# Optimization experiments

Measured on AMD Instinct MI355X. Metric: run time of the kernel, lower is better.

Reference implementation:

```python
import jax, jax.numpy as jnp
import numpy as np

H = 56; W = 56; WS = 7; SS = 3; NH = 6; C = 192; B = 32
T = H * W; HD = C // NH; NW = (H // WS) * (W // WS); TW = WS * WS
SCALE = HD ** -0.5


def _rel_index():
    # relative position index per WindowAttentionLayer.calculate_coordinates
    coords = np.stack(np.meshgrid(np.arange(WS), np.arange(WS), indexing='ij')).reshape(2, -1)
    rel = (coords[:, :, None] - coords[:, None, :]).transpose(1, 2, 0).astype(np.int64)
    rel[:, :, 0] += WS - 1
    rel[:, :, 1] += WS - 1
    rel[:, :, 0] *= 2 * WS - 1
    return rel.sum(-1).reshape(-1)  # [TW*TW]


def _attn_mask():
    # shifted-window attention mask, per WindowAttentionBlock.__init__
    img = np.zeros((H, W))
    slices = (slice(0, -WS), slice(-WS, -SS), slice(-SS, None))
    cnt = 0
    for hs in slices:
        for ws_ in slices:
            img[hs, ws_] = cnt
            cnt += 1
    mw = img.reshape(H // WS, WS, W // WS, WS).transpose(0, 2, 1, 3).reshape(-1, TW)
    am = mw[:, None, :] - mw[:, :, None]
    return np.where(am != 0, np.float32(-100.0), np.float32(0.0))  # [NW, TW, TW]


_REL = jnp.asarray(_rel_index())
_MASK = jnp.asarray(_attn_mask())


def _ln(x, g, b):
    m = x.mean(-1, keepdims=True)
    v = ((x - m) ** 2).mean(-1, keepdims=True)
    return (x - m) * jax.lax.rsqrt(v + 1e-5) * g + b


def setup_inputs() -> dict:
    key = jax.random.key(0)
    ks = jax.random.split(key, 8)
    s = 0.02
    return {
        'x': jax.random.normal(ks[0], (B, T, C), jnp.float32),
        'ln1_g': jnp.ones((C,), jnp.float32),
        'ln1_b': jnp.zeros((C,), jnp.float32),
        'qkv_w': jax.random.normal(ks[1], (C, 3 * C), jnp.float32) * s,
        'qkv_b': jnp.zeros((3 * C,), jnp.float32),
        'pos_bias': jax.random.normal(ks[2], ((2 * WS - 1) * (2 * WS - 1), NH), jnp.float32) * s,
        'proj_w': jax.random.normal(ks[3], (C, C), jnp.float32) * s,
        'proj_b': jnp.zeros((C,), jnp.float32),
        'ln2_g': jnp.ones((C,), jnp.float32),
        'ln2_b': jnp.zeros((C,), jnp.float32),
        'mlp_w1': jax.random.normal(ks[4], (C, 4 * C), jnp.float32) * s,
        'mlp_b1': jnp.zeros((4 * C,), jnp.float32),
        'mlp_w2': jax.random.normal(ks[5], (4 * C, C), jnp.float32) * s,
        'mlp_b2': jnp.zeros((C,), jnp.float32),
    }


def reference(x, ln1_g, ln1_b, qkv_w, qkv_b, pos_bias, proj_w, proj_b,
              ln2_g, ln2_b, mlp_w1, mlp_b1, mlp_w2, mlp_b2):
    shortcut = x
    h = _ln(x, ln1_g, ln1_b).reshape(B, H, W, C)
    h = jnp.roll(h, (-SS, -SS), axis=(1, 2))  # cyclic shift
    # window partition -> [B*NW, TW, C]
    h = h.reshape(B, H // WS, WS, W // WS, WS, C).transpose(0, 1, 3, 2, 4, 5).reshape(B * NW, TW, C)
    qkv = (h @ qkv_w + qkv_b).reshape(B * NW, TW, 3, NH, HD).transpose(2, 0, 3, 1, 4)
    q, k, v = qkv[0] * SCALE, qkv[1], qkv[2]  # [B*NW, NH, TW, HD]
    attn = jnp.einsum('nhid,nhjd->nhij', q, k)  # [B*NW, NH, TW, TW]
    bias = pos_bias[_REL].reshape(TW, TW, NH).transpose(2, 0, 1)  # [NH, TW, TW]
    attn = attn + bias[None]
    attn = (attn.reshape(B, NW, NH, TW, TW) + _MASK[None, :, None]).reshape(B * NW, NH, TW, TW)
    # NOTE: the source forward never applies softmax (self.softmax is unused) -- replicated faithfully
    o = jnp.einsum('nhij,nhjd->nhid', attn, v).transpose(0, 2, 1, 3).reshape(B * NW, TW, C)
    o = o @ proj_w + proj_b
    # window reverse + reverse shift
    o = o.reshape(B, H // WS, W // WS, WS, WS, C).transpose(0, 1, 3, 2, 4, 5).reshape(B, H, W, C)
    o = jnp.roll(o, (SS, SS), axis=(1, 2)).reshape(B, T, C)
    x1 = shortcut + o
    m = _ln(x1, ln2_g, ln2_b)
    m = jax.nn.gelu(m @ mlp_w1 + mlp_b1, approximate=False) @ mlp_w2 + mlp_b2
    return x1 + m
```

## Files before the change

### kernel.cpp

```cpp
#include <hip/hip_runtime.h>
#include <hip/hip_bf16.h>

typedef __attribute__((ext_vector_type(8))) short short8;
typedef __attribute__((ext_vector_type(4))) float floatx4;

#define SCALE_Q 0.17677669529663687f

__device__ __forceinline__ short f2bf(float f) {
  union { float f; unsigned u; } a; a.f = f;
  unsigned r = (a.u + 0x7FFFu + ((a.u >> 16) & 1u)) >> 16;
  return (short)r;
}

__global__ void transpose_w_k(const float* __restrict__ src, short* __restrict__ dst,
                              int K, int N) {
  int i = blockIdx.x * 256 + threadIdx.x;
  if (i >= N * K) return;
  int n = i / K, k = i - n * K;
  dst[i] = f2bf(src[(size_t)k * N + n]);
}

__global__ void prep_bm_k(const float* __restrict__ pos_bias, float* __restrict__ bm) {
  int i = blockIdx.x * 256 + threadIdx.x;
  if (i >= 64 * 6 * 49 * 49) return;
  int j = i % 49; int t = i / 49; int ii = t % 49; t /= 49; int h = t % 6; int w = t / 6;
  int ih = ii / 7, iw = ii - ih * 7, jh = j / 7, jw = j - jh * 7;
  int rel = (ih - jh + 6) * 13 + (iw - jw + 6);
  float v = pos_bias[rel * 6 + h];
  int wh = w >> 3, ww = w & 7;
  int ri = wh * 7 + ih, ci = ww * 7 + iw, rj = wh * 7 + jh, cj = ww * 7 + jw;
  int regi = ((ri >= 49) + (ri >= 53)) * 3 + ((ci >= 49) + (ci >= 53));
  int regj = ((rj >= 49) + (rj >= 53)) * 3 + ((cj >= 49) + (cj >= 53));
  if (regi != regj) v -= 100.0f;
  bm[i] = v;
}

template<int SHIFT>
__global__ __launch_bounds__(256) void ln_k(const float* __restrict__ x,
    const float* __restrict__ g, const float* __restrict__ bta,
    short* __restrict__ outb) {
  int wid = threadIdx.x >> 6, lane = threadIdx.x & 63;
  int r = blockIdx.x * 4 + wid;
  size_t src;
  if (SHIFT) {
    int n = r / 49, tw = r - n * 49;
    int bb = n >> 6, wdx = n & 63;
    int rh = (wdx >> 3) * 7 + tw / 7, rw = (wdx & 7) * 7 + tw % 7;
    int sh = rh + 3; if (sh >= 56) sh -= 56;
    int sw = rw + 3; if (sw >= 56) sw -= 56;
    src = ((size_t)bb * 3136 + sh * 56 + sw) * 192;
  } else {
    src = (size_t)r * 192;
  }
  const float* xr = x + src;
  float v0 = xr[lane], v1 = xr[lane + 64], v2 = xr[lane + 128];
  float s = v0 + v1 + v2, sq = v0 * v0 + v1 * v1 + v2 * v2;
  #pragma unroll
  for (int o = 32; o >= 1; o >>= 1) { s += __shfl_xor(s, o); sq += __shfl_xor(sq, o); }
  float mean = s * (1.0f / 192.0f);
  float rstd = rsqrtf(sq * (1.0f / 192.0f) - mean * mean + 1e-5f);
  short* orow = outb + (size_t)r * 192;
  orow[lane]       = f2bf((v0 - mean) * rstd * g[lane]       + bta[lane]);
  orow[lane + 64]  = f2bf((v1 - mean) * rstd * g[lane + 64]  + bta[lane + 64]);
  orow[lane + 128] = f2bf((v2 - mean) * rstd * g[lane + 128] + bta[lane + 128]);
}

template<int EPI>
__global__ __launch_bounds__(256) void gemm_k(
    const short* __restrict__ A, const short* __restrict__ Bt,
    const float* __restrict__ bias, void* __restrict__ outp,
    const void* __restrict__ aux, int N, int K) {
  __shared__ short As[128][72];
  __shared__ short Bs[64][72];
  int tid = threadIdx.x;
  int gmb = blockIdx.y * 128;
  int gnb = blockIdx.x * 64;
  int wid = tid >> 6, lane = tid & 63;
  int wm = wid >> 1, wn = wid & 1;
  int lr = lane & 15, lk = (lane >> 4) << 3, lq = (lane >> 4) << 2;
  floatx4 acc[4][2];
  #pragma unroll
  for (int i = 0; i < 4; ++i)
    #pragma unroll
    for (int j = 0; j < 2; ++j) acc[i][j] = (floatx4)(0.0f);

  for (int k0 = 0; k0 < K; k0 += 64) {
    #pragma unroll
    for (int i = 0; i < 4; ++i) {
      int u = tid + 256 * i;
      int row = u >> 3, cb = (u & 7) << 3;
      *(short8*)&As[row][cb] = *(const short8*)&A[(size_t)(gmb + row) * K + k0 + cb];
    }
    #pragma unroll
    for (int i = 0; i < 2; ++i) {
      int u = tid + 256 * i;
      int row = u >> 3, cb = (u & 7) << 3;
      *(short8*)&Bs[row][cb] = *(const short8*)&Bt[(size_t)(gnb + row) * K + k0 + cb];
    }
    __syncthreads();
    #pragma unroll
    for (int kk = 0; kk < 64; kk += 32) {
      short8 af[4], bfr[2];
      #pragma unroll
      for (int mi = 0; mi < 4; ++mi)
        af[mi] = *(const short8*)&As[wm * 64 + mi * 16 + lr][kk + lk];
      #pragma unroll
      for (int ni = 0; ni < 2; ++ni)
        bfr[ni] = *(const short8*)&Bs[wn * 32 + ni * 16 + lr][kk + lk];
      #pragma unroll
      for (int mi = 0; mi < 4; ++mi)
        #pragma unroll
        for (int ni = 0; ni < 2; ++ni)
          acc[mi][ni] = __builtin_amdgcn_mfma_f32_16x16x32_bf16(af[mi], bfr[ni], acc[mi][ni], 0, 0, 0);
    }
    __syncthreads();
  }

  #pragma unroll
  for (int mi = 0; mi < 4; ++mi) {
    #pragma unroll
    for (int ni = 0; ni < 2; ++ni) {
      #pragma unroll
      for (int r = 0; r < 4; ++r) {
        int grow = gmb + wm * 64 + mi * 16 + lq + r;
        int gcol = gnb + wn * 32 + ni * 16 + lr;
        float v = acc[mi][ni][r] + bias[gcol];
        if (EPI == 0) {
          int which = gcol / 192, rem = gcol - which * 192;
          if (which == 0) v *= SCALE_Q;
          int head = rem >> 5, d = rem & 31;
          int n = grow / 49, tw = grow - n * 49;
          ((short*)outp)[((((size_t)(n * 6 + head) * 3 + which) * 49 + tw) << 5) + d] = f2bf(v);
        } else if (EPI == 1) {
          int n = grow / 49, tw = grow - n * 49;
          int bb = n >> 6, wdx = n & 63;
          int rh = (wdx >> 3) * 7 + tw / 7, rw = (wdx & 7) * 7 + tw % 7;
          int oh = rh + 3; if (oh >= 56) oh -= 56;
          int ow = rw + 3; if (ow >= 56) ow -= 56;
          size_t idx = ((size_t)bb * 3136 + oh * 56 + ow) * 192 + gcol;
          ((float*)outp)[idx] = ((const float*)aux)[idx] + v;
        } else if (EPI == 2) {
          float ge = 0.5f * v * (1.0f + erff(v * 0.70710678118f));
          ((short*)outp)[(size_t)grow * 768 + gcol] = f2bf(ge);
        } else {
          size_t idx = (size_t)grow * 192 + gcol;
          ((float*)outp)[idx] += v;
        }
      }
    }
  }
}

__global__ __launch_bounds__(256) void attn_k(const short* __restrict__ qkv,
    const float* __restrict__ bm, short* __restrict__ obuf) {
  __shared__ short lds[4][6912];
  int wid = threadIdx.x >> 6, lane = threadIdx.x & 63;
  int pair = blockIdx.x * 4 + wid;
  int n = pair / 6, h = pair - n * 6;
  short* Vt = &lds[wid][0];
  short* Ps = &lds[wid][32 * 72];
  const short* Qb = qkv + (size_t)((n * 6 + h) * 3) * 1568;
  const short* Kb = Qb + 1568;
  const short* Vb = Qb + 3136;
  int lr = lane & 15, lk = (lane >> 4) << 3, lq = (lane >> 4) << 2;

  #pragma unroll
  for (int it = 0; it < 8; ++it) {
    int u = lane + 64 * it;
    Vt[(u >> 4) * 72 + 48 + (u & 15)] = 0;
  }
  #pragma unroll
  for (int it = 0; it < 4; ++it) {
    int u = lane + 64 * it;
    if (u < 196) {
      int tw = u >> 2, db = (u & 3) << 3;
      short8 vv = *(const short8*)&Vb[tw * 32 + db];
      #pragma unroll
      for (int j = 0; j < 8; ++j) Vt[(db + j) * 72 + tw] = vv[j];
    }
  }

  short8 qf[4], kf[4];
  #pragma unroll
  for (int mi = 0; mi < 4; ++mi)
    qf[mi] = *(const short8*)&Qb[(mi * 16 + lr) * 32 + lk];
  #pragma unroll
  for (int nj = 0; nj < 4; ++nj)
    kf[nj] = *(const short8*)&Kb[(nj * 16 + lr) * 32 + lk];
  floatx4 s[4][4];
  #pragma unroll
  for (int mi = 0; mi < 4; ++mi)
    #pragma unroll
    for (int nj = 0; nj < 4; ++nj)
      s[mi][nj] = __builtin_amdgcn_mfma_f32_16x16x32_bf16(qf[mi], kf[nj], (floatx4)(0.0f), 0, 0, 0);

  const float* bmw = bm + (size_t)((n & 63) * 6 + h) * 2401;
  #pragma unroll
  for (int mi = 0; mi < 4; ++mi)
    #pragma unroll
    for (int nj = 0; nj < 4; ++nj)
      #pragma unroll
      for (int r = 0; r < 4; ++r) {
        int i = mi * 16 + lq + r;
        int j = nj * 16 + lr;
        float v = 0.0f;
        if (i < 49 && j < 49) v = s[mi][nj][r] + bmw[i * 49 + j];
        Ps[i * 72 + j] = f2bf(v);
      }

  floatx4 o[4][2];
  #pragma unroll
  for (int mi = 0; mi < 4; ++mi)
    #pragma unroll
    for (int ni = 0; ni < 2; ++ni) o[mi][ni] = (floatx4)(0.0f);
  #pragma unroll
  for (int kc = 0; kc < 2; ++kc) {
    short8 pf[4], vf[2];
    #pragma unroll
    for (int mi = 0; mi < 4; ++mi)
      pf[mi] = *(const short8*)&Ps[(mi * 16 + lr) * 72 + kc * 32 + lk];
    #pragma unroll
    for (int ni = 0; ni < 2; ++ni)
      vf[ni] = *(const short8*)&Vt[(ni * 16 + lr) * 72 + kc * 32 + lk];
    #pragma unroll
    for (int mi = 0; mi < 4; ++mi)
      #pragma unroll
      for (int ni = 0; ni < 2; ++ni)
        o[mi][ni] = __builtin_amdgcn_mfma_f32_16x16x32_bf16(pf[mi], vf[ni], o[mi][ni], 0, 0, 0);
  }
  #pragma unroll
  for (int mi = 0; mi < 4; ++mi)
    #pragma unroll
    for (int ni = 0; ni < 2; ++ni)
      #pragma unroll
      for (int r = 0; r < 4; ++r) {
        int i = mi * 16 + lq + r;
        if (i < 49)
          obuf[((size_t)n * 49 + i) * 192 + h * 32 + ni * 16 + lr] = f2bf(o[mi][ni][r]);
      }
}

extern "C" void kernel_launch(void* const* d_in, const int* in_sizes, int n_in,
                              void* d_out, int out_size, void* d_ws, size_t ws_size,
                              hipStream_t stream) {
  const float* x      = (const float*)d_in[0];
  const float* ln1_g  = (const float*)d_in[1];
  const float* ln1_b  = (const float*)d_in[2];
  const float* qkv_w  = (const float*)d_in[3];
  const float* qkv_b  = (const float*)d_in[4];
  const float* pos_b  = (const float*)d_in[5];
  const float* proj_w = (const float*)d_in[6];
  const float* proj_b = (const float*)d_in[7];
  const float* ln2_g  = (const float*)d_in[8];
  const float* ln2_b  = (const float*)d_in[9];
  const float* mlp_w1 = (const float*)d_in[10];
  const float* mlp_b1 = (const float*)d_in[11];
  const float* mlp_w2 = (const float*)d_in[12];
  const float* mlp_b2 = (const float*)d_in[13];

  char* ws = (char*)d_ws;
  short* qkvbuf  = (short*)(ws);
  short* obuf    = (short*)(ws + 115605504);
  short* hidden  = (short*)(ws);
  short* hbuf    = (short*)(ws + 154140672);
  short* wT      = (short*)(ws + 192675840);
  short* qkv_wT  = wT;
  short* proj_wT = wT + 110592;
  short* m1_wT   = wT + 110592 + 36864;
  short* m2_wT   = wT + 110592 + 36864 + 147456;
  float* bm      = (float*)(ws + 193560576);
  float* xout    = (float*)d_out;

  transpose_w_k<<<(110592 + 255) / 256, 256, 0, stream>>>(qkv_w,  qkv_wT, 192, 576);
  transpose_w_k<<<(36864  + 255) / 256, 256, 0, stream>>>(proj_w, proj_wT, 192, 192);
  transpose_w_k<<<(147456 + 255) / 256, 256, 0, stream>>>(mlp_w1, m1_wT,  192, 768);
  transpose_w_k<<<(147456 + 255) / 256, 256, 0, stream>>>(mlp_w2, m2_wT,  768, 192);
  prep_bm_k<<<(64 * 6 * 2401 + 255) / 256, 256, 0, stream>>>(pos_b, bm);

  ln_k<1><<<25088, 256, 0, stream>>>(x, ln1_g, ln1_b, hbuf);
  gemm_k<0><<<dim3(9, 784),  256, 0, stream>>>(hbuf, qkv_wT, qkv_b, qkvbuf, nullptr, 576, 192);
  attn_k<<<3072, 256, 0, stream>>>(qkvbuf, bm, obuf);
  gemm_k<1><<<dim3(3, 784),  256, 0, stream>>>(obuf, proj_wT, proj_b, xout, x, 192, 192);
  ln_k<0><<<25088, 256, 0, stream>>>(xout, ln2_g, ln2_b, hbuf);
  gemm_k<2><<<dim3(12, 784), 256, 0, stream>>>(hbuf, m1_wT, mlp_b1, hidden, nullptr, 768, 192);
  gemm_k<3><<<dim3(3, 784),  256, 0, stream>>>(hidden, m2_wT, mlp_b2, xout, nullptr, 192, 768);
}
```

Baseline: 507.0 us.

## Fuse projection, residual, LayerNorm2 and MLP into one per-tile tail kernel

Replaces the proj GEMM, second LayerNorm, MLP1 GEMM and MLP2 GEMM with a single kernel that processes 128 window-ordered rows per block. The hidden activation is kept in LDS in 64-column chunks and is never written to global memory. The residual, LN statistics and final output all use the shifted-window spatial row mapping, which removes the x1 round trip and three kernel launches. In exchange, operands are read straight from global memory with no LDS staging for the weights. Each block also gets only 784 blocks of 512 threads, which may limit occupancy and weight reuse.

```diff
diff --git a/kernel.cpp b/kernel.cpp
--- a/kernel.cpp
+++ b/kernel.cpp
@@ -10,6 +10,15 @@
   union { float f; unsigned u; } a; a.f = f;
   unsigned r = (a.u + 0x7FFFu + ((a.u >> 16) & 1u)) >> 16;
   return (short)r;
+}
+
+__device__ __forceinline__ int spatial_row(int r) {
+  int n = r / 49, tw = r - n * 49;
+  int bb = n >> 6, wdx = n & 63;
+  int rh = (wdx >> 3) * 7 + tw / 7, rw = (wdx & 7) * 7 + tw % 7;
+  int oh = rh + 3; if (oh >= 56) oh -= 56;
+  int ow = rw + 3; if (ow >= 56) ow -= 56;
+  return bb * 3136 + oh * 56 + ow;
 }
 
 __global__ void transpose_w_k(const float* __restrict__ src, short* __restrict__ dst,
@@ -35,23 +44,17 @@
   bm[i] = v;
 }
 
-template<int SHIFT>
 __global__ __launch_bounds__(256) void ln_k(const float* __restrict__ x,
     const float* __restrict__ g, const float* __restrict__ bta,
     short* __restrict__ outb) {
   int wid = threadIdx.x >> 6, lane = threadIdx.x & 63;
   int r = blockIdx.x * 4 + wid;
-  size_t src;
-  if (SHIFT) {
-    int n = r / 49, tw = r - n * 49;
-    int bb = n >> 6, wdx = n & 63;
-    int rh = (wdx >> 3) * 7 + tw / 7, rw = (wdx & 7) * 7 + tw % 7;
-    int sh = rh + 3; if (sh >= 56) sh -= 56;
-    int sw = rw + 3; if (sw >= 56) sw -= 56;
-    src = ((size_t)bb * 3136 + sh * 56 + sw) * 192;
-  } else {
-    src = (size_t)r * 192;
-  }
+  int n = r / 49, tw = r - n * 49;
+  int bb = n >> 6, wdx = n & 63;
+  int rh = (wdx >> 3) * 7 + tw / 7, rw = (wdx & 7) * 7 + tw % 7;
+  int sh = rh + 3; if (sh >= 56) sh -= 56;
+  int sw = rw + 3; if (sw >= 56) sw -= 56;
+  size_t src = ((size_t)bb * 3136 + sh * 56 + sw) * 192;
   const float* xr = x + src;
   float v0 = xr[lane], v1 = xr[lane + 64], v2 = xr[lane + 128];
   float s = v0 + v1 + v2, sq = v0 * v0 + v1 * v1 + v2 * v2;
@@ -65,11 +68,9 @@
   orow[lane + 128] = f2bf((v2 - mean) * rstd * g[lane + 128] + bta[lane + 128]);
 }
 
-template<int EPI>
-__global__ __launch_bounds__(256) void gemm_k(
+__global__ __launch_bounds__(256) void gemm_qkv_k(
     const short* __restrict__ A, const short* __restrict__ Bt,
-    const float* __restrict__ bias, void* __restrict__ outp,
-    const void* __restrict__ aux, int N, int K) {
+    const float* __restrict__ bias, short* __restrict__ outp, int N, int K) {
   __shared__ short As[128][72];
   __shared__ short Bs[64][72];
   int tid = threadIdx.x;
@@ -117,38 +118,20 @@
   }
 
   #pragma unroll
-  for (int mi = 0; mi < 4; ++mi) {
-    #pragma unroll
-    for (int ni = 0; ni < 2; ++ni) {
+  for (int mi = 0; mi < 4; ++mi)
+    #pragma unroll
+    for (int ni = 0; ni < 2; ++ni)
       #pragma unroll
       for (int r = 0; r < 4; ++r) {
         int grow = gmb + wm * 64 + mi * 16 + lq + r;
         int gcol = gnb + wn * 32 + ni * 16 + lr;
         float v = acc[mi][ni][r] + bias[gcol];
-        if (EPI == 0) {
-          int which = gcol / 192, rem = gcol - which * 192;
-          if (which == 0) v *= SCALE_Q;
-          int head = rem >> 5, d = rem & 31;
-          int n = grow / 49, tw = grow - n * 49;
-          ((short*)outp)[((((size_t)(n * 6 + head) * 3 + which) * 49 + tw) << 5) + d] = f2bf(v);
-        } else if (EPI == 1) {
-          int n = grow / 49, tw = grow - n * 49;
-          int bb = n >> 6, wdx = n & 63;
-          int rh = (wdx >> 3) * 7 + tw / 7, rw = (wdx & 7) * 7 + tw % 7;
-          int oh = rh + 3; if (oh >= 56) oh -= 56;
-          int ow = rw + 3; if (ow >= 56) ow -= 56;
-          size_t idx = ((size_t)bb * 3136 + oh * 56 + ow) * 192 + gcol;
-          ((float*)outp)[idx] = ((const float*)aux)[idx] + v;
-        } else if (EPI == 2) {
-          float ge = 0.5f * v * (1.0f + erff(v * 0.70710678118f));
-          ((short*)outp)[(size_t)grow * 768 + gcol] = f2bf(ge);
-        } else {
-          size_t idx = (size_t)grow * 192 + gcol;
-          ((float*)outp)[idx] += v;
-        }
+        int which = gcol / 192, rem = gcol - which * 192;
+        if (which == 0) v *= SCALE_Q;
+        int head = rem >> 5, d = rem & 31;
+        int n = grow / 49, tw = grow - n * 49;
+        outp[((((size_t)(n * 6 + head) * 3 + which) * 49 + tw) << 5) + d] = f2bf(v);
       }
-    }
-  }
 }
 
 __global__ __launch_bounds__(256) void attn_k(const short* __restrict__ qkv,
@@ -238,6 +221,155 @@
         if (i < 49)
           obuf[((size_t)n * 49 + i) * 192 + h * 32 + ni * 16 + lr] = f2bf(o[mi][ni][r]);
       }
+}
+
+__global__ __launch_bounds__(512, 2) void tail_k(
+    const short* __restrict__ obuf, const short* __restrict__ projT,
+    const float* __restrict__ proj_b, const float* __restrict__ x,
+    const float* __restrict__ g2, const float* __restrict__ bt2,
+    const short* __restrict__ w1T, const float* __restrict__ b1,
+    const short* __restrict__ w2T, const float* __restrict__ b2,
+    float* __restrict__ out) {
+  __shared__ short As[128][200];
+  __shared__ short Hc[128][72];
+  __shared__ float sums[128][4][2];
+  __shared__ float stats[128][2];
+
+  int tid = threadIdx.x;
+  int wid = tid >> 6, lane = tid & 63;
+  int wm = wid >> 2, wn = wid & 3;
+  int lr = lane & 15, lk = (lane >> 4) << 3, lq = (lane >> 4) << 2;
+  int blk = blockIdx.x * 128;
+
+  floatx4 acc[4][3];
+  #pragma unroll
+  for (int mi = 0; mi < 4; ++mi)
+    #pragma unroll
+    for (int ni = 0; ni < 3; ++ni) acc[mi][ni] = (floatx4)(0.0f);
+  #pragma unroll
+  for (int kk = 0; kk < 6; ++kk) {
+    short8 af[4], bfr[3];
+    #pragma unroll
+    for (int mi = 0; mi < 4; ++mi)
+      af[mi] = *(const short8*)&obuf[(size_t)(blk + wm * 64 + mi * 16 + lr) * 192 + kk * 32 + lk];
+    #pragma unroll
+    for (int ni = 0; ni < 3; ++ni)
+      bfr[ni] = *(const short8*)&projT[(size_t)(wn * 48 + ni * 16 + lr) * 192 + kk * 32 + lk];
+    #pragma unroll
+    for (int mi = 0; mi < 4; ++mi)
+      #pragma unroll
+      for (int ni = 0; ni < 3; ++ni)
+        acc[mi][ni] = __builtin_amdgcn_mfma_f32_16x16x32_bf16(af[mi], bfr[ni], acc[mi][ni], 0, 0, 0);
+  }
+
+  float pb[3], gv[3], bv[3], pb2[3];
+  int col[3];
+  #pragma unroll
+  for (int ni = 0; ni < 3; ++ni) {
+    col[ni] = wn * 48 + ni * 16 + lr;
+    pb[ni] = proj_b[col[ni]];
+    gv[ni] = g2[col[ni]];
+    bv[ni] = bt2[col[ni]];
+    pb2[ni] = b2[col[ni]];
+  }
+
+  int srw[4][4];
+  #pragma unroll
+  for (int mi = 0; mi < 4; ++mi) {
+    #pragma unroll
+    for (int rr = 0; rr < 4; ++rr) {
+      int row_l = wm * 64 + mi * 16 + lq + rr;
+      int sr = spatial_row(blk + row_l);
+      srw[mi][rr] = sr;
+      float s = 0.0f, sq = 0.0f;
+      #pragma unroll
+      for (int ni = 0; ni < 3; ++ni) {
+        float v = acc[mi][ni][rr] + pb[ni] + x[(size_t)sr * 192 + col[ni]];
+        acc[mi][ni][rr] = v;
+        s += v; sq += v * v;
+      }
+      #pragma unroll
+      for (int o = 8; o >= 1; o >>= 1) { s += __shfl_xor(s, o); sq += __shfl_xor(sq, o); }
+      if (lr == 0) { sums[row_l][wn][0] = s; sums[row_l][wn][1] = sq; }
+    }
+  }
+  __syncthreads();
+  if (tid < 128) {
+    float s = sums[tid][0][0] + sums[tid][1][0] + sums[tid][2][0] + sums[tid][3][0];
+    float sq = sums[tid][0][1] + sums[tid][1][1] + sums[tid][2][1] + sums[tid][3][1];
+    float mean = s * (1.0f / 192.0f);
+    float var = sq * (1.0f / 192.0f) - mean * mean;
+    stats[tid][0] = mean;
+    stats[tid][1] = rsqrtf(var + 1e-5f);
+  }
+  __syncthreads();
+
+  #pragma unroll
+  for (int mi = 0; mi < 4; ++mi)
+    #pragma unroll
+    for (int rr = 0; rr < 4; ++rr) {
+      int row_l = wm * 64 + mi * 16 + lq + rr;
+      float mean = stats[row_l][0], rstd = stats[row_l][1];
+      #pragma unroll
+      for (int ni = 0; ni < 3; ++ni)
+        As[row_l][col[ni]] = f2bf((acc[mi][ni][rr] - mean) * rstd * gv[ni] + bv[ni]);
+    }
+  __syncthreads();
+
+  int hcol = wn * 16 + lr;
+  for (int c = 0; c < 12; ++c) {
+    floatx4 hacc[4];
+    #pragma unroll
+    for (int mi = 0; mi < 4; ++mi) hacc[mi] = (floatx4)(0.0f);
+    const short* w1p = w1T + (size_t)(c * 64 + hcol) * 192;
+    #pragma unroll
+    for (int kk = 0; kk < 6; ++kk) {
+      short8 bfr = *(const short8*)&w1p[kk * 32 + lk];
+      short8 af[4];
+      #pragma unroll
+      for (int mi = 0; mi < 4; ++mi)
+        af[mi] = *(const short8*)&As[wm * 64 + mi * 16 + lr][kk * 32 + lk];
+      #pragma unroll
+      for (int mi = 0; mi < 4; ++mi)
+        hacc[mi] = __builtin_amdgcn_mfma_f32_16x16x32_bf16(af[mi], bfr, hacc[mi], 0, 0, 0);
+    }
+    float b1v = b1[c * 64 + hcol];
+    #pragma unroll
+    for (int mi = 0; mi < 4; ++mi)
+      #pragma unroll
+      for (int rr = 0; rr < 4; ++rr) {
+        float hv = hacc[mi][rr] + b1v;
+        float ge = 0.5f * hv * (1.0f + erff(hv * 0.70710678118f));
+        Hc[wm * 64 + mi * 16 + lq + rr][hcol] = f2bf(ge);
+      }
+    __syncthreads();
+    #pragma unroll
+    for (int kk = 0; kk < 2; ++kk) {
+      short8 af[4], bfr[3];
+      #pragma unroll
+      for (int mi = 0; mi < 4; ++mi)
+        af[mi] = *(const short8*)&Hc[wm * 64 + mi * 16 + lr][kk * 32 + lk];
+      #pragma unroll
+      for (int ni = 0; ni < 3; ++ni)
+        bfr[ni] = *(const short8*)&w2T[(size_t)col[ni] * 768 + c * 64 + kk * 32 + lk];
+      #pragma unroll
+      for (int mi = 0; mi < 4; ++mi)
+        #pragma unroll
+        for (int ni = 0; ni < 3; ++ni)
+          acc[mi][ni] = __builtin_amdgcn_mfma_f32_16x16x32_bf16(af[mi], bfr[ni], acc[mi][ni], 0, 0, 0);
+    }
+    __syncthreads();
+  }
+
+  #pragma unroll
+  for (int mi = 0; mi < 4; ++mi)
+    #pragma unroll
+    for (int rr = 0; rr < 4; ++rr) {
+      int sr = srw[mi][rr];
+      #pragma unroll
+      for (int ni = 0; ni < 3; ++ni)
+        out[(size_t)sr * 192 + col[ni]] = acc[mi][ni][rr] + pb2[ni];
+    }
 }
 
 extern "C" void kernel_launch(void* const* d_in, const int* in_sizes, int n_in,
@@ -261,7 +393,6 @@
   char* ws = (char*)d_ws;
   short* qkvbuf  = (short*)(ws);
   short* obuf    = (short*)(ws + 115605504);
-  short* hidden  = (short*)(ws);
   short* hbuf    = (short*)(ws + 154140672);
   short* wT      = (short*)(ws + 192675840);
   short* qkv_wT  = wT;
@@ -277,11 +408,9 @@
   transpose_w_k<<<(147456 + 255) / 256, 256, 0, stream>>>(mlp_w2, m2_wT,  768, 192);
   prep_bm_k<<<(64 * 6 * 2401 + 255) / 256, 256, 0, stream>>>(pos_b, bm);
 
-  ln_k<1><<<25088, 256, 0, stream>>>(x, ln1_g, ln1_b, hbuf);
-  gemm_k<0><<<dim3(9, 784),  256, 0, stream>>>(hbuf, qkv_wT, qkv_b, qkvbuf, nullptr, 576, 192);
+  ln_k<<<25088, 256, 0, stream>>>(x, ln1_g, ln1_b, hbuf);
+  gemm_qkv_k<<<dim3(9, 784), 256, 0, stream>>>(hbuf, qkv_wT, qkv_b, qkvbuf, 576, 192);
   attn_k<<<3072, 256, 0, stream>>>(qkvbuf, bm, obuf);
-  gemm_k<1><<<dim3(3, 784),  256, 0, stream>>>(obuf, proj_wT, proj_b, xout, x, 192, 192);
-  ln_k<0><<<25088, 256, 0, stream>>>(xout, ln2_g, ln2_b, hbuf);
-  gemm_k<2><<<dim3(12, 784), 256, 0, stream>>>(hbuf, m1_wT, mlp_b1, hidden, nullptr, 768, 192);
-  gemm_k<3><<<dim3(3, 784),  256, 0, stream>>>(hidden, m2_wT, mlp_b2, xout, nullptr, 192, 768);
-}
+  tail_k<<<784, 512, 0, stream>>>(obuf, proj_wT, proj_b, x, ln2_g, ln2_b,
+                                  m1_wT, mlp_b1, m2_wT, mlp_b2, xout);
+}
```

Result: slower. 576.3 us (+13.7%).
